# Performance work log

Hardware: AMD Instinct MI355X
Metric: run time of the kernel (lower is better)

Reference implementation:

```python
import jax, jax.numpy as jnp
import numpy as np

B, P, E, D, A = 128, 196, 2048, 512, 512


def setup_inputs() -> dict:
    key = jax.random.key(0)
    ks = jax.random.split(key, 8)
    s = lambda fan_in: 1.0 / np.sqrt(fan_in)
    return {
        "encoder_out": jax.random.normal(ks[0], (B, P, E), jnp.float32),
        "decoder_hidden": jax.random.normal(ks[1], (B, D), jnp.float32),
        "We": jax.random.uniform(ks[2], (E, A), jnp.float32, -s(E), s(E)),
        "be": jax.random.uniform(ks[3], (A,), jnp.float32, -s(E), s(E)),
        "Wd": jax.random.uniform(ks[4], (D, A), jnp.float32, -s(D), s(D)),
        "bd": jax.random.uniform(ks[5], (A,), jnp.float32, -s(D), s(D)),
        "Wf": jax.random.uniform(ks[6], (A, 1), jnp.float32, -s(A), s(A)),
        "bf": jax.random.uniform(ks[7], (1,), jnp.float32, -s(A), s(A)),
    }


def reference(encoder_out, decoder_hidden, We, be, Wd, bd, Wf, bf):
    # att1: [B, P, A]
    att1 = jnp.einsum("bpe,ea->bpa", encoder_out, We) + be
    # att2: [B, A]
    att2 = decoder_hidden @ Wd + bd
    # additive attention scores: [B, P]
    att = (jax.nn.relu(att1 + att2[:, None, :]) @ Wf + bf)[..., 0]
    alpha = jax.nn.softmax(att, axis=1)  # softmax over pixels
    # weighted sum over pixels: [B, E]
    awe = jnp.einsum("bpe,bp->be", encoder_out, alpha)
    return awe, alpha
```

## Files before the change

### kernel.cpp

```cpp
#include <hip/hip_runtime.h>
#include <hip/hip_bf16.h>

typedef __attribute__((ext_vector_type(2))) unsigned int u32x2;
typedef __attribute__((ext_vector_type(4))) float f32x4;
typedef __attribute__((ext_vector_type(4))) unsigned int u32x4;
typedef __attribute__((ext_vector_type(8))) short s16x8;

#define B_  128
#define P_  196
#define E_  2048
#define D_  512
#define A_  512
#define M_  (B_*P_)

typedef __attribute__((address_space(1))) const unsigned int gu32;
typedef __attribute__((address_space(3))) unsigned int lu32;
__device__ __forceinline__ void gl_lds16(const void* g, void* l) {
  __builtin_amdgcn_global_load_lds((gu32*)g, (lu32*)l, 16, 0, 0);
}

#define WAIT_VM3() asm volatile("s_waitcnt vmcnt(3)" ::: "memory")
#define WAIT_VM0() asm volatile("s_waitcnt vmcnt(0)" ::: "memory")
#define WAIT_LGKM0() asm volatile("s_waitcnt lgkmcnt(0)" ::: "memory")

__global__ void we_conv_kernel(const float* __restrict__ We,
                               unsigned short* __restrict__ WeTs) {
  __shared__ float tile[32][33];
  const int tx = threadIdx.x, ty = threadIdx.y;
  const int a0 = blockIdx.x * 32, e0 = blockIdx.y * 32;
  tile[ty][tx] = We[(e0 + ty) * A_ + a0 + tx];
  __syncthreads();
  const float v = tile[tx][ty];
  const unsigned int u = __float_as_uint(v);
  const unsigned short r = (unsigned short)((u + 0x7fffu + ((u >> 16) & 1u)) >> 16);
  const int a = a0 + ty;
  const int kt = blockIdx.y;
  const int c8 = tx >> 3, j = tx & 7;
  const int dest = ((a * 32 + c8 * 8) ^ ((a & 7) << 3)) + j;
  WeTs[kt * 16384 + dest] = r;
}

__global__ void att2_kernel(const float* __restrict__ h, const float* __restrict__ Wd,
                            const float* __restrict__ bd, const float* __restrict__ be,
                            float* __restrict__ att2pb) {
  const int b = blockIdx.x;
  const int t = threadIdx.x;
  __shared__ float hs[D_];
  hs[t] = h[b * D_ + t];
  hs[t + 256] = h[b * D_ + t + 256];
  __syncthreads();
  float a0 = 0.f, a1 = 0.f;
  for (int d = 0; d < D_; ++d) {
    const float hv = hs[d];
    a0 = fmaf(hv, Wd[d * A_ + t], a0);
    a1 = fmaf(hv, Wd[d * A_ + t + 256], a1);
  }
  att2pb[b * A_ + t] = a0 + bd[t] + be[t];
  att2pb[b * A_ + t + 256] = a1 + bd[t + 256] + be[t + 256];
}

__device__ inline unsigned pk2(float a, float b) {
  union { __hip_bfloat162 h; unsigned u; } cv;
  cv.h = __float22bfloat162_rn(make_float2(a, b));
  return cv.u;
}

__launch_bounds__(1024, 4)
__global__ void score_kernel(const float* __restrict__ enc,
                             const unsigned short* __restrict__ WeTs,
                             const float* __restrict__ att2pb,
                             const float* __restrict__ Wf,
                             float* __restrict__ att_part) {
  __shared__ unsigned short Bh[3][512 * 32];
  __shared__ unsigned short Ahs[3][128 * 32];

  const int bid = blockIdx.x;
  const int m0 = bid * 128;

  const int t = threadIdx.x;
  const int lane = t & 63, w = t >> 6;
  const int wm = (w >> 2) * 32;
  const int wn = (w & 3) * 128;

  const int ar = t >> 3, ac4 = t & 7;
  const float* aptr = enc + (size_t)(m0 + ar) * E_ + ac4 * 4;
  const int awz = (ar * 32 + ac4 * 4) ^ ((ar & 7) << 3);

  const int doff = t * 8;

  const int q = lane >> 4, fr = lane & 15;
  const int fx = (fr & 7) << 3;
  int fa[2], fb[8];
#pragma unroll
  for (int i = 0; i < 2; ++i) fa[i] = ((wm + i * 16 + fr) * 32 + q * 8) ^ fx;
#pragma unroll
  for (int j = 0; j < 8; ++j) fb[j] = ((wn + j * 16 + fr) * 32 + q * 8) ^ fx;

  const f32x4 zero = {0.f, 0.f, 0.f, 0.f};
  f32x4 acc[2][8];
#pragma unroll
  for (int mi = 0; mi < 2; ++mi)
#pragma unroll
    for (int ni = 0; ni < 8; ++ni) acc[mi][ni] = zero;

  unsigned short *bAc = &Ahs[0][0], *bA1 = &Ahs[1][0], *bA2 = &Ahs[2][0];
  unsigned short *bBc = &Bh[0][0],  *bB1 = &Bh[1][0],  *bB2 = &Bh[2][0];

  f32x4 aC, aN;

  {
    aC = *(const f32x4*)(aptr);
    gl_lds16(WeTs + doff, bBc + doff);
    gl_lds16(WeTs + 8192 + doff, bBc + 8192 + doff);
    aN = *(const f32x4*)(aptr + 32);
    gl_lds16(WeTs + 16384 + doff, bB1 + doff);
    gl_lds16(WeTs + 16384 + 8192 + doff, bB1 + 8192 + doff);
    u32x2 av; av[0] = pk2(aC[0], aC[1]); av[1] = pk2(aC[2], aC[3]);
    *(u32x2*)(bAc + awz) = av;
    aC = aN;
    WAIT_VM3();
    WAIT_LGKM0();
    __builtin_amdgcn_s_barrier();
  }

  for (int it = 0; it < 62; ++it) {
    const int kof = (it + 2) * 32;
    aN = *(const f32x4*)(aptr + kof);
    const unsigned short* sb = WeTs + (size_t)(it + 2) * 16384;
    gl_lds16(sb + doff, bB2 + doff);
    gl_lds16(sb + 8192 + doff, bB2 + 8192 + doff);

    s16x8 fah[2], fbh[4];
    fah[0] = *(const s16x8*)(bAc + fa[0]);
    fah[1] = *(const s16x8*)(bAc + fa[1]);
#pragma unroll
    for (int j = 0; j < 4; ++j) fbh[j] = *(const s16x8*)(bBc + fb[j]);
    __builtin_amdgcn_s_setprio(1);
#pragma unroll
    for (int mi = 0; mi < 2; ++mi)
#pragma unroll
      for (int ni = 0; ni < 4; ++ni)
        acc[mi][ni] = __builtin_amdgcn_mfma_f32_16x16x32_bf16(fah[mi], fbh[ni], acc[mi][ni], 0, 0, 0);
    __builtin_amdgcn_s_setprio(0);
#pragma unroll
    for (int j = 0; j < 4; ++j) fbh[j] = *(const s16x8*)(bBc + fb[4 + j]);
    __builtin_amdgcn_s_setprio(1);
#pragma unroll
    for (int mi = 0; mi < 2; ++mi)
#pragma unroll
      for (int ni = 0; ni < 4; ++ni)
        acc[mi][4 + ni] = __builtin_amdgcn_mfma_f32_16x16x32_bf16(fah[mi], fbh[ni], acc[mi][4 + ni], 0, 0, 0);
    __builtin_amdgcn_s_setprio(0);

    {
      u32x2 av; av[0] = pk2(aC[0], aC[1]); av[1] = pk2(aC[2], aC[3]);
      *(u32x2*)(bA1 + awz) = av;
    }
    aC = aN;

    WAIT_VM3();
    WAIT_LGKM0();
    __builtin_amdgcn_s_barrier();

    unsigned short* tmp;
    tmp = bAc; bAc = bA1; bA1 = bA2; bA2 = tmp;
    tmp = bBc; bBc = bB1; bB1 = bB2; bB2 = tmp;
  }

  {
    s16x8 fah[2], fbh[4];
    fah[0] = *(const s16x8*)(bAc + fa[0]);
    fah[1] = *(const s16x8*)(bAc + fa[1]);
#pragma unroll
    for (int j = 0; j < 4; ++j) fbh[j] = *(const s16x8*)(bBc + fb[j]);
#pragma unroll
    for (int mi = 0; mi < 2; ++mi)
#pragma unroll
      for (int ni = 0; ni < 4; ++ni)
        acc[mi][ni] = __builtin_amdgcn_mfma_f32_16x16x32_bf16(fah[mi], fbh[ni], acc[mi][ni], 0, 0, 0);
#pragma unroll
    for (int j = 0; j < 4; ++j) fbh[j] = *(const s16x8*)(bBc + fb[4 + j]);
#pragma unroll
    for (int mi = 0; mi < 2; ++mi)
#pragma unroll
      for (int ni = 0; ni < 4; ++ni)
        acc[mi][4 + ni] = __builtin_amdgcn_mfma_f32_16x16x32_bf16(fah[mi], fbh[ni], acc[mi][4 + ni], 0, 0, 0);
    u32x2 av; av[0] = pk2(aC[0], aC[1]); av[1] = pk2(aC[2], aC[3]);
    *(u32x2*)(bA1 + awz) = av;
    WAIT_VM0();
    WAIT_LGKM0();
    __builtin_amdgcn_s_barrier();
  }

  {
    s16x8 fah[2], fbh[4];
    fah[0] = *(const s16x8*)(bA1 + fa[0]);
    fah[1] = *(const s16x8*)(bA1 + fa[1]);
#pragma unroll
    for (int j = 0; j < 4; ++j) fbh[j] = *(const s16x8*)(bB1 + fb[j]);
#pragma unroll
    for (int mi = 0; mi < 2; ++mi)
#pragma unroll
      for (int ni = 0; ni < 4; ++ni)
        acc[mi][ni] = __builtin_amdgcn_mfma_f32_16x16x32_bf16(fah[mi], fbh[ni], acc[mi][ni], 0, 0, 0);
#pragma unroll
    for (int j = 0; j < 4; ++j) fbh[j] = *(const s16x8*)(bB1 + fb[4 + j]);
#pragma unroll
    for (int mi = 0; mi < 2; ++mi)
#pragma unroll
      for (int ni = 0; ni < 4; ++ni)
        acc[mi][4 + ni] = __builtin_amdgcn_mfma_f32_16x16x32_bf16(fah[mi], fbh[ni], acc[mi][4 + ni], 0, 0, 0);
  }

  const int colL = wn + fr;
  float wfv[8];
#pragma unroll
  for (int ni = 0; ni < 8; ++ni) wfv[ni] = Wf[colL + ni * 16];
#pragma unroll
  for (int mi = 0; mi < 2; ++mi) {
    const int rowb = m0 + wm + mi * 16 + (q << 2);
#pragma unroll
    for (int r = 0; r < 4; ++r) {
      const int row = rowb + r;
      const int bb = row / P_;
      const float* a2 = att2pb + bb * A_ + colL;
      float s = 0.f;
#pragma unroll
      for (int ni = 0; ni < 8; ++ni)
        s += fmaxf(acc[mi][ni][r] + a2[ni * 16], 0.f) * wfv[ni];
#pragma unroll
      for (int off = 1; off < 16; off <<= 1) s += __shfl_xor(s, off);
      if (fr == 0) att_part[row * 4 + (w & 3)] = s;
    }
  }
}

__global__ void softmax_awe_kernel(const float* __restrict__ enc,
                                   const float* __restrict__ att_part,
                                   float* __restrict__ out) {
  const int bid = blockIdx.x;
  const int b = bid >> 1, ch = bid & 1;
  const int t = threadIdx.x;
  __shared__ float sm[256];
  __shared__ float alpha_s[P_];

  float av = -1e30f;
  if (t < P_) {
    const float* apt = att_part + (b * P_ + t) * 4;
    av = (apt[0] + apt[1]) + (apt[2] + apt[3]);
  }
  sm[t] = av;
  __syncthreads();
  for (int st = 128; st > 0; st >>= 1) {
    if (t < st) sm[t] = fmaxf(sm[t], sm[t + st]);
    __syncthreads();
  }
  const float mx = sm[0];
  __syncthreads();
  float ev = 0.f;
  if (t < P_) ev = __expf(av - mx);
  sm[t] = ev;
  __syncthreads();
  for (int st = 128; st > 0; st >>= 1) {
    if (t < st) sm[t] += sm[t + st];
    __syncthreads();
  }
  const float denom = sm[0];
  const float al = ev / denom;
  if (t < P_) {
    alpha_s[t] = al;
    if (ch == 0) out[B_ * E_ + b * P_ + t] = al;
  }
  __syncthreads();

  const int e0 = ch * 1024 + t * 4;
  const float* ebase = enc + (size_t)b * P_ * E_ + e0;
  f32x4 acc = {0.f, 0.f, 0.f, 0.f};
  for (int p = 0; p < P_; ++p) {
    const f32x4 v = *(const f32x4*)(ebase + (size_t)p * E_);
    const float a = alpha_s[p];
    acc.x += a * v.x; acc.y += a * v.y; acc.z += a * v.z; acc.w += a * v.w;
  }
  *(f32x4*)(out + b * E_ + e0) = acc;
}

extern "C" void kernel_launch(void* const* d_in, const int* in_sizes, int n_in,
                              void* d_out, int out_size, void* d_ws, size_t ws_size,
                              hipStream_t stream) {
  const float* enc = (const float*)d_in[0];
  const float* h   = (const float*)d_in[1];
  const float* We  = (const float*)d_in[2];
  const float* be  = (const float*)d_in[3];
  const float* Wd  = (const float*)d_in[4];
  const float* bd  = (const float*)d_in[5];
  const float* Wf  = (const float*)d_in[6];
  float* out = (float*)d_out;

  float* att2pb = (float*)d_ws;
  float* att_part = att2pb + B_ * A_;
  unsigned short* WeTs = (unsigned short*)(att_part + M_ * 4);

  we_conv_kernel<<<dim3(A_ / 32, E_ / 32), dim3(32, 32), 0, stream>>>(We, WeTs);
  att2_kernel<<<B_, 256, 0, stream>>>(h, Wd, bd, be, att2pb);
  score_kernel<<<M_ / 128, 1024, 0, stream>>>(enc, WeTs, att2pb, Wf, att_part);
  softmax_awe_kernel<<<B_ * 2, 256, 0, stream>>>(enc, att_part, out);
}
```

Measured before the change: 130.3 us.

## Use square 64x64 warp tiles and a 4-deep B-tile prefetch pipeline

Warps are rearranged from a 4x4 grid of 32x128 tiles into a 2x8 grid of 64x64 tiles, which balances the A and B fragment loads from LDS per MFMA. The B (WeTs) LDS buffering grows from 3 to 4 stages, fetched three tiles ahead, while A drops to double buffering; the vmcnt waits and epilogue are adjusted to match. Because each row now receives 8 partial scores instead of 4, att_part doubles in size and the softmax kernel sums 8 partials. LDS use per block grows, and the wait counts and ring indices must stay exactly right.

```diff
diff --git a/kernel.cpp b/kernel.cpp
--- a/kernel.cpp
+++ b/kernel.cpp
@@ -19,7 +19,9 @@
   __builtin_amdgcn_global_load_lds((gu32*)g, (lu32*)l, 16, 0, 0);
 }
 
-#define WAIT_VM3() asm volatile("s_waitcnt vmcnt(3)" ::: "memory")
+#define WAIT_VM6() asm volatile("s_waitcnt vmcnt(6)" ::: "memory")
+#define WAIT_VM5() asm volatile("s_waitcnt vmcnt(5)" ::: "memory")
+#define WAIT_VM4() asm volatile("s_waitcnt vmcnt(4)" ::: "memory")
 #define WAIT_VM0() asm volatile("s_waitcnt vmcnt(0)" ::: "memory")
 #define WAIT_LGKM0() asm volatile("s_waitcnt lgkmcnt(0)" ::: "memory")
 
@@ -71,16 +73,16 @@
                              const float* __restrict__ att2pb,
                              const float* __restrict__ Wf,
                              float* __restrict__ att_part) {
-  __shared__ unsigned short Bh[3][512 * 32];
-  __shared__ unsigned short Ahs[3][128 * 32];
+  __shared__ unsigned short Bh[4][512 * 32];
+  __shared__ unsigned short Ahs[2][128 * 32];
 
   const int bid = blockIdx.x;
   const int m0 = bid * 128;
 
   const int t = threadIdx.x;
   const int lane = t & 63, w = t >> 6;
-  const int wm = (w >> 2) * 32;
-  const int wn = (w & 3) * 128;
+  const int wm = (w >> 3) * 64;
+  const int wn = (w & 7) * 64;
 
   const int ar = t >> 3, ac4 = t & 7;
   const float* aptr = enc + (size_t)(m0 + ar) * E_ + ac4 * 4;
@@ -90,134 +92,118 @@
 
   const int q = lane >> 4, fr = lane & 15;
   const int fx = (fr & 7) << 3;
-  int fa[2], fb[8];
-#pragma unroll
-  for (int i = 0; i < 2; ++i) fa[i] = ((wm + i * 16 + fr) * 32 + q * 8) ^ fx;
-#pragma unroll
-  for (int j = 0; j < 8; ++j) fb[j] = ((wn + j * 16 + fr) * 32 + q * 8) ^ fx;
+  int fa[4], fb[4];
+#pragma unroll
+  for (int i = 0; i < 4; ++i) {
+    fa[i] = ((wm + i * 16 + fr) * 32 + q * 8) ^ fx;
+    fb[i] = ((wn + i * 16 + fr) * 32 + q * 8) ^ fx;
+  }
 
   const f32x4 zero = {0.f, 0.f, 0.f, 0.f};
-  f32x4 acc[2][8];
-#pragma unroll
-  for (int mi = 0; mi < 2; ++mi)
-#pragma unroll
-    for (int ni = 0; ni < 8; ++ni) acc[mi][ni] = zero;
-
-  unsigned short *bAc = &Ahs[0][0], *bA1 = &Ahs[1][0], *bA2 = &Ahs[2][0];
-  unsigned short *bBc = &Bh[0][0],  *bB1 = &Bh[1][0],  *bB2 = &Bh[2][0];
+  f32x4 acc[4][4];
+#pragma unroll
+  for (int mi = 0; mi < 4; ++mi)
+#pragma unroll
+    for (int ni = 0; ni < 4; ++ni) acc[mi][ni] = zero;
 
   f32x4 aC, aN;
 
   {
     aC = *(const f32x4*)(aptr);
-    gl_lds16(WeTs + doff, bBc + doff);
-    gl_lds16(WeTs + 8192 + doff, bBc + 8192 + doff);
+    gl_lds16(WeTs + doff, &Bh[0][doff]);
+    gl_lds16(WeTs + 8192 + doff, &Bh[0][8192 + doff]);
     aN = *(const f32x4*)(aptr + 32);
-    gl_lds16(WeTs + 16384 + doff, bB1 + doff);
-    gl_lds16(WeTs + 16384 + 8192 + doff, bB1 + 8192 + doff);
+    gl_lds16(WeTs + 16384 + doff, &Bh[1][doff]);
+    gl_lds16(WeTs + 16384 + 8192 + doff, &Bh[1][8192 + doff]);
+    gl_lds16(WeTs + 32768 + doff, &Bh[2][doff]);
+    gl_lds16(WeTs + 32768 + 8192 + doff, &Bh[2][8192 + doff]);
     u32x2 av; av[0] = pk2(aC[0], aC[1]); av[1] = pk2(aC[2], aC[3]);
-    *(u32x2*)(bAc + awz) = av;
+    *(u32x2*)(&Ahs[0][awz]) = av;
     aC = aN;
-    WAIT_VM3();
-    WAIT_LGKM0();
-    __builtin_amdgcn_s_barrier();
-  }
-
-  for (int it = 0; it < 62; ++it) {
+    WAIT_VM5();
+    WAIT_LGKM0();
+    __builtin_amdgcn_s_barrier();
+  }
+
+#define COMPUTE_TILE(AB, BB)                                                     \
+  {                                                                              \
+    s16x8 fah[4], fbh[2];                                                        \
+    fah[0] = *(const s16x8*)((AB) + fa[0]);                                      \
+    fah[1] = *(const s16x8*)((AB) + fa[1]);                                      \
+    fah[2] = *(const s16x8*)((AB) + fa[2]);                                      \
+    fah[3] = *(const s16x8*)((AB) + fa[3]);                                      \
+    fbh[0] = *(const s16x8*)((BB) + fb[0]);                                      \
+    fbh[1] = *(const s16x8*)((BB) + fb[1]);                                      \
+    __builtin_amdgcn_s_setprio(1);                                               \
+    _Pragma("unroll")                                                            \
+    for (int mi = 0; mi < 4; ++mi) {                                             \
+      acc[mi][0] = __builtin_amdgcn_mfma_f32_16x16x32_bf16(fah[mi], fbh[0], acc[mi][0], 0, 0, 0); \
+      acc[mi][1] = __builtin_amdgcn_mfma_f32_16x16x32_bf16(fah[mi], fbh[1], acc[mi][1], 0, 0, 0); \
+    }                                                                            \
+    __builtin_amdgcn_s_setprio(0);                                               \
+    fbh[0] = *(const s16x8*)((BB) + fb[2]);                                      \
+    fbh[1] = *(const s16x8*)((BB) + fb[3]);                                      \
+    __builtin_amdgcn_s_setprio(1);                                               \
+    _Pragma("unroll")                                                            \
+    for (int mi = 0; mi < 4; ++mi) {                                             \
+      acc[mi][2] = __builtin_amdgcn_mfma_f32_16x16x32_bf16(fah[mi], fbh[0], acc[mi][2], 0, 0, 0); \
+      acc[mi][3] = __builtin_amdgcn_mfma_f32_16x16x32_bf16(fah[mi], fbh[1], acc[mi][3], 0, 0, 0); \
+    }                                                                            \
+    __builtin_amdgcn_s_setprio(0);                                               \
+  }
+
+  for (int it = 0; it < 61; ++it) {
     const int kof = (it + 2) * 32;
     aN = *(const f32x4*)(aptr + kof);
-    const unsigned short* sb = WeTs + (size_t)(it + 2) * 16384;
-    gl_lds16(sb + doff, bB2 + doff);
-    gl_lds16(sb + 8192 + doff, bB2 + 8192 + doff);
-
-    s16x8 fah[2], fbh[4];
-    fah[0] = *(const s16x8*)(bAc + fa[0]);
-    fah[1] = *(const s16x8*)(bAc + fa[1]);
-#pragma unroll
-    for (int j = 0; j < 4; ++j) fbh[j] = *(const s16x8*)(bBc + fb[j]);
-    __builtin_amdgcn_s_setprio(1);
-#pragma unroll
-    for (int mi = 0; mi < 2; ++mi)
-#pragma unroll
-      for (int ni = 0; ni < 4; ++ni)
-        acc[mi][ni] = __builtin_amdgcn_mfma_f32_16x16x32_bf16(fah[mi], fbh[ni], acc[mi][ni], 0, 0, 0);
-    __builtin_amdgcn_s_setprio(0);
-#pragma unroll
-    for (int j = 0; j < 4; ++j) fbh[j] = *(const s16x8*)(bBc + fb[4 + j]);
-    __builtin_amdgcn_s_setprio(1);
-#pragma unroll
-    for (int mi = 0; mi < 2; ++mi)
-#pragma unroll
-      for (int ni = 0; ni < 4; ++ni)
-        acc[mi][4 + ni] = __builtin_amdgcn_mfma_f32_16x16x32_bf16(fah[mi], fbh[ni], acc[mi][4 + ni], 0, 0, 0);
-    __builtin_amdgcn_s_setprio(0);
+    {
+      const unsigned short* sb = WeTs + (size_t)(it + 3) * 16384;
+      unsigned short* bt = &Bh[(it + 3) & 3][0];
+      gl_lds16(sb + doff, bt + doff);
+      gl_lds16(sb + 8192 + doff, bt + 8192 + doff);
+    }
+
+    COMPUTE_TILE(&Ahs[it & 1][0], &Bh[it & 3][0])
 
     {
       u32x2 av; av[0] = pk2(aC[0], aC[1]); av[1] = pk2(aC[2], aC[3]);
-      *(u32x2*)(bA1 + awz) = av;
+      *(u32x2*)(&Ahs[(it + 1) & 1][awz]) = av;
     }
     aC = aN;
 
-    WAIT_VM3();
-    WAIT_LGKM0();
-    __builtin_amdgcn_s_barrier();
-
-    unsigned short* tmp;
-    tmp = bAc; bAc = bA1; bA1 = bA2; bA2 = tmp;
-    tmp = bBc; bBc = bB1; bB1 = bB2; bB2 = tmp;
+    WAIT_VM6();
+    WAIT_LGKM0();
+    __builtin_amdgcn_s_barrier();
   }
 
   {
-    s16x8 fah[2], fbh[4];
-    fah[0] = *(const s16x8*)(bAc + fa[0]);
-    fah[1] = *(const s16x8*)(bAc + fa[1]);
-#pragma unroll
-    for (int j = 0; j < 4; ++j) fbh[j] = *(const s16x8*)(bBc + fb[j]);
-#pragma unroll
-    for (int mi = 0; mi < 2; ++mi)
-#pragma unroll
-      for (int ni = 0; ni < 4; ++ni)
-        acc[mi][ni] = __builtin_amdgcn_mfma_f32_16x16x32_bf16(fah[mi], fbh[ni], acc[mi][ni], 0, 0, 0);
-#pragma unroll
-    for (int j = 0; j < 4; ++j) fbh[j] = *(const s16x8*)(bBc + fb[4 + j]);
-#pragma unroll
-    for (int mi = 0; mi < 2; ++mi)
-#pragma unroll
-      for (int ni = 0; ni < 4; ++ni)
-        acc[mi][4 + ni] = __builtin_amdgcn_mfma_f32_16x16x32_bf16(fah[mi], fbh[ni], acc[mi][4 + ni], 0, 0, 0);
+    aN = *(const f32x4*)(aptr + 63 * 32);
+    COMPUTE_TILE(&Ahs[1][0], &Bh[1][0])
     u32x2 av; av[0] = pk2(aC[0], aC[1]); av[1] = pk2(aC[2], aC[3]);
-    *(u32x2*)(bA1 + awz) = av;
+    *(u32x2*)(&Ahs[0][awz]) = av;
+    aC = aN;
+    WAIT_VM4();
+    WAIT_LGKM0();
+    __builtin_amdgcn_s_barrier();
+  }
+
+  {
+    COMPUTE_TILE(&Ahs[0][0], &Bh[2][0])
+    u32x2 av; av[0] = pk2(aC[0], aC[1]); av[1] = pk2(aC[2], aC[3]);
+    *(u32x2*)(&Ahs[1][awz]) = av;
     WAIT_VM0();
     WAIT_LGKM0();
     __builtin_amdgcn_s_barrier();
   }
 
-  {
-    s16x8 fah[2], fbh[4];
-    fah[0] = *(const s16x8*)(bA1 + fa[0]);
-    fah[1] = *(const s16x8*)(bA1 + fa[1]);
-#pragma unroll
-    for (int j = 0; j < 4; ++j) fbh[j] = *(const s16x8*)(bB1 + fb[j]);
-#pragma unroll
-    for (int mi = 0; mi < 2; ++mi)
-#pragma unroll
-      for (int ni = 0; ni < 4; ++ni)
-        acc[mi][ni] = __builtin_amdgcn_mfma_f32_16x16x32_bf16(fah[mi], fbh[ni], acc[mi][ni], 0, 0, 0);
-#pragma unroll
-    for (int j = 0; j < 4; ++j) fbh[j] = *(const s16x8*)(bB1 + fb[4 + j]);
-#pragma unroll
-    for (int mi = 0; mi < 2; ++mi)
-#pragma unroll
-      for (int ni = 0; ni < 4; ++ni)
-        acc[mi][4 + ni] = __builtin_amdgcn_mfma_f32_16x16x32_bf16(fah[mi], fbh[ni], acc[mi][4 + ni], 0, 0, 0);
-  }
+  COMPUTE_TILE(&Ahs[1][0], &Bh[3][0])
+#undef COMPUTE_TILE
 
   const int colL = wn + fr;
-  float wfv[8];
-#pragma unroll
-  for (int ni = 0; ni < 8; ++ni) wfv[ni] = Wf[colL + ni * 16];
-#pragma unroll
-  for (int mi = 0; mi < 2; ++mi) {
+  float wfv[4];
+#pragma unroll
+  for (int ni = 0; ni < 4; ++ni) wfv[ni] = Wf[colL + ni * 16];
+#pragma unroll
+  for (int mi = 0; mi < 4; ++mi) {
     const int rowb = m0 + wm + mi * 16 + (q << 2);
 #pragma unroll
     for (int r = 0; r < 4; ++r) {
@@ -226,11 +212,11 @@
       const float* a2 = att2pb + bb * A_ + colL;
       float s = 0.f;
 #pragma unroll
-      for (int ni = 0; ni < 8; ++ni)
+      for (int ni = 0; ni < 4; ++ni)
         s += fmaxf(acc[mi][ni][r] + a2[ni * 16], 0.f) * wfv[ni];
 #pragma unroll
       for (int off = 1; off < 16; off <<= 1) s += __shfl_xor(s, off);
-      if (fr == 0) att_part[row * 4 + (w & 3)] = s;
+      if (fr == 0) att_part[row * 8 + (w & 7)] = s;
     }
   }
 }
@@ -246,8 +232,11 @@
 
   float av = -1e30f;
   if (t < P_) {
-    const float* apt = att_part + (b * P_ + t) * 4;
-    av = (apt[0] + apt[1]) + (apt[2] + apt[3]);
+    const float* apt = att_part + (b * P_ + t) * 8;
+    float s = 0.f;
+#pragma unroll
+    for (int i = 0; i < 8; ++i) s += apt[i];
+    av = s;
   }
   sm[t] = av;
   __syncthreads();
@@ -298,7 +287,7 @@
 
   float* att2pb = (float*)d_ws;
   float* att_part = att2pb + B_ * A_;
-  unsigned short* WeTs = (unsigned short*)(att_part + M_ * 4);
+  unsigned short* WeTs = (unsigned short*)(att_part + M_ * 8);
 
   we_conv_kernel<<<dim3(A_ / 32, E_ / 32), dim3(32, 32), 0, stream>>>(We, WeTs);
   att2_kernel<<<B_, 256, 0, stream>>>(h, Wd, bd, be, att2pb);
```

Result: slower. 143.5 us (+10.1%).
